# Optimization experiments

Hardware: AMD Instinct MI355X
Metric: run time of the kernel (lower is better)

## Reference

```python
import jax, jax.numpy as jnp
import numpy as np

N_NODES = 1_000_000
N_EDGES = 16_000_000
F_IN, F_H1, F_H2, N_CLS = 32, 16, 8, 5
N_GRAPHS = 10_000


def setup_inputs() -> dict:
    key = jax.random.key(0)
    ks = jax.random.split(key, 10)
    x = jax.random.normal(ks[0], (N_NODES, F_IN), dtype=jnp.float32)
    edge_index = jax.random.randint(ks[1], (2, N_EDGES), 0, N_NODES, dtype=jnp.int32)
    batch = jnp.sort(jax.random.randint(ks[2], (N_NODES,), 0, N_GRAPHS, dtype=jnp.int32))
    # learned params (Glorot-ish scale)
    W1 = jax.random.normal(ks[3], (F_IN, F_H1), dtype=jnp.float32) / np.sqrt(F_IN)
    b1 = jnp.zeros((F_H1,), dtype=jnp.float32)
    W2 = jax.random.normal(ks[4], (F_H1, F_H2), dtype=jnp.float32) / np.sqrt(F_H1)
    b2 = jnp.zeros((F_H2,), dtype=jnp.float32)
    Wl = jax.random.normal(ks[5], (F_H2, N_CLS), dtype=jnp.float32) / np.sqrt(F_H2)
    bl = jnp.zeros((N_CLS,), dtype=jnp.float32)
    return {"x": x, "edge_index": edge_index, "batch": batch, "num_graphs": N_GRAPHS,
            "W1": W1, "b1": b1, "W2": W2, "b2": b2, "Wl": Wl, "bl": bl}


def _gcn_conv(x, W, b, src, dst, deg_inv_sqrt, norm_e, num_nodes):
    # h = X W, then symmetric-normalized aggregation with self loops:
    # out_i = sum_{(j->i)} norm_ji * h_j + deg_i^{-1} * h_i + b
    h = x @ W                                  # [N, F_out]
    msg = h[src] * norm_e[:, None]             # [E, F_out] gather + scale
    agg = jax.ops.segment_sum(msg, dst, num_segments=num_nodes)
    self_loop = h * (deg_inv_sqrt * deg_inv_sqrt)[:, None]
    return agg + self_loop + b


def reference(x, edge_index, batch, num_graphs, W1, b1, W2, b2, Wl, bl):
    num_nodes = x.shape[0]
    src, dst = edge_index[0], edge_index[1]
    # degrees including self loops (GCN: A_hat = A + I)
    deg = jax.ops.segment_sum(jnp.ones_like(dst, dtype=x.dtype), dst,
                              num_segments=num_nodes) + 1.0
    deg_inv_sqrt = jax.lax.rsqrt(deg)
    norm_e = deg_inv_sqrt[src] * deg_inv_sqrt[dst]   # [E]

    h = _gcn_conv(x, W1, b1, src, dst, deg_inv_sqrt, norm_e, num_nodes)
    h = jax.nn.relu(h)
    h = _gcn_conv(h, W2, b2, src, dst, deg_inv_sqrt, norm_e, num_nodes)
    h = jax.nn.relu(h)

    # global_mean_pool over graph ids
    sums = jax.ops.segment_sum(h, batch, num_segments=num_graphs)     # [G, F_H2]
    cnts = jax.ops.segment_sum(jnp.ones((num_nodes,), dtype=h.dtype), batch,
                               num_segments=num_graphs)
    pooled = sums / jnp.maximum(cnts, 1.0)[:, None]
    return pooled @ Wl + bl
```

## Files before the change

### kernel.cpp

```cpp
#include <hip/hip_runtime.h>


namespace {

constexpr int F_IN = 32, F_H1 = 16, F_H2 = 8, N_CLS = 5;
constexpr int BB = 10, NPB = 1 << BB;
constexpr int MAXB = 1024;
constexpr int CHUNK = 12288;


__global__ void k_mm1(const float* __restrict__ x, const float* __restrict__ W,
                      const float* __restrict__ dis, float* __restrict__ h, int N) {
  __shared__ float w[F_IN * F_H1];
  for (int k = threadIdx.x; k < F_IN * F_H1; k += blockDim.x) w[k] = W[k];
  __syncthreads();
  int i = blockIdx.x * blockDim.x + threadIdx.x;
  if (i >= N) return;
  const float4* xr = reinterpret_cast<const float4*>(x + (size_t)i * F_IN);
  float acc[F_H1];
#pragma unroll
  for (int f = 0; f < F_H1; ++f) acc[f] = 0.f;
#pragma unroll
  for (int k4 = 0; k4 < F_IN / 4; ++k4) {
    float4 v = xr[k4];
    float vv[4] = {v.x, v.y, v.z, v.w};
#pragma unroll
    for (int j = 0; j < 4; ++j) {
      const float* wr = &w[(k4 * 4 + j) * F_H1];
#pragma unroll
      for (int f = 0; f < F_H1; ++f) acc[f] = fmaf(vv[j], wr[f], acc[f]);
    }
  }
  float s = dis ? dis[i] : 1.0f;
  float4* hr = reinterpret_cast<float4*>(h + (size_t)i * F_H1);
#pragma unroll
  for (int q = 0; q < F_H1 / 4; ++q)
    hr[q] = make_float4(s * acc[q * 4], s * acc[q * 4 + 1], s * acc[q * 4 + 2],
                        s * acc[q * 4 + 3]);
}

__global__ void k_mm2(const float* __restrict__ in, const float* __restrict__ W,
                      const float* __restrict__ dis, float* __restrict__ h, int N) {
  __shared__ float w[F_H1 * F_H2];
  for (int k = threadIdx.x; k < F_H1 * F_H2; k += blockDim.x) w[k] = W[k];
  __syncthreads();
  int i = blockIdx.x * blockDim.x + threadIdx.x;
  if (i >= N) return;
  const float4* xr = reinterpret_cast<const float4*>(in + (size_t)i * F_H1);
  float acc[F_H2];
#pragma unroll
  for (int f = 0; f < F_H2; ++f) acc[f] = 0.f;
#pragma unroll
  for (int k4 = 0; k4 < F_H1 / 4; ++k4) {
    float4 v = xr[k4];
    float vv[4] = {v.x, v.y, v.z, v.w};
#pragma unroll
    for (int j = 0; j < 4; ++j) {
      const float* wr = &w[(k4 * 4 + j) * F_H2];
#pragma unroll
      for (int f = 0; f < F_H2; ++f) acc[f] = fmaf(vv[j], wr[f], acc[f]);
    }
  }
  float s = dis ? dis[i] : 1.0f;
  float4* hr = reinterpret_cast<float4*>(h + (size_t)i * F_H2);
#pragma unroll
  for (int q = 0; q < F_H2 / 4; ++q)
    hr[q] = make_float4(s * acc[q * 4], s * acc[q * 4 + 1], s * acc[q * 4 + 2],
                        s * acc[q * 4 + 3]);
}

__global__ void k_final(const float* __restrict__ pooled, const float* __restrict__ cnts,
                        const float* __restrict__ Wl, const float* __restrict__ bl,
                        float* __restrict__ out, int total) {
  int gid = blockIdx.x * blockDim.x + threadIdx.x;
  if (gid >= total) return;
  int g = gid / N_CLS, c = gid % N_CLS;
  float s = 0.f;
#pragma unroll
  for (int f = 0; f < F_H2; ++f) s += pooled[g * F_H2 + f] * Wl[f * N_CLS + c];
  out[gid] = s / fmaxf(cnts[g], 1.f) + bl[c];
}


__global__ void k_hist(const int* __restrict__ dst, int* __restrict__ bcnt,
                       int E, int nbuck) {
  __shared__ int h[MAXB];
  for (int i = threadIdx.x; i < MAXB; i += blockDim.x) h[i] = 0;
  __syncthreads();
  for (int e = blockIdx.x * blockDim.x + threadIdx.x; e < E;
       e += gridDim.x * blockDim.x)
    atomicAdd(&h[dst[e] >> BB], 1);
  __syncthreads();
  for (int i = threadIdx.x; i < nbuck; i += blockDim.x)
    if (h[i]) atomicAdd(&bcnt[i], h[i]);
}

__global__ void k_bscan(const int* __restrict__ bcnt, int* __restrict__ bbase,
                        int* __restrict__ bcur, int nbuck, int E) {
  __shared__ int s[MAXB];
  int t = threadIdx.x;
  int v = (t < nbuck) ? bcnt[t] : 0;
  s[t] = v;
  __syncthreads();
  for (int off = 1; off < MAXB; off <<= 1) {
    int x = (t >= off) ? s[t - off] : 0;
    __syncthreads();
    s[t] += x;
    __syncthreads();
  }
  int ex = s[t] - v;
  if (t < nbuck) { bbase[t] = ex; bcur[t] = ex; }
  if (t == 0) bbase[nbuck] = E;
}

__global__ __launch_bounds__(256)
void k_binscatter(const int* __restrict__ dst, const int* __restrict__ src,
                  int* __restrict__ bcur, int* __restrict__ packed, int E) {
  __shared__ int hist[MAXB];
  __shared__ int sbase[MAXB];
  __shared__ int lcur[MAXB];
  __shared__ int stg[CHUNK];
  __shared__ int stmp[256];
  int t = threadIdx.x;
  int c0 = blockIdx.x * CHUNK;
  int n = min(CHUNK, E - c0);
  for (int i = t; i < MAXB; i += 256) hist[i] = 0;
  __syncthreads();
  for (int j = t; j < n; j += 256) atomicAdd(&hist[dst[c0 + j] >> BB], 1);
  __syncthreads();
  int v[4], sum = 0;
  int b4 = t * 4;
#pragma unroll
  for (int k = 0; k < 4; ++k) { v[k] = hist[b4 + k]; sum += v[k]; }
  stmp[t] = sum;
  __syncthreads();
  for (int off = 1; off < 256; off <<= 1) {
    int x = (t >= off) ? stmp[t - off] : 0;
    __syncthreads();
    stmp[t] += x;
    __syncthreads();
  }
  int run = stmp[t] - sum;
#pragma unroll
  for (int k = 0; k < 4; ++k) { sbase[b4 + k] = run; lcur[b4 + k] = run; run += v[k]; }
  __syncthreads();
  for (int i = t; i < MAXB; i += 256) {
    int c = hist[i];
    if (c) hist[i] = atomicAdd(&bcur[i], c);
  }
  __syncthreads();
  for (int j = t; j < n; j += 256) {
    int d = dst[c0 + j], s = src[c0 + j];
    int b = d >> BB;
    int p = atomicAdd(&lcur[b], 1);
    stg[p] = ((d & (NPB - 1)) << 20) | s;
  }
  __syncthreads();
  for (int j = t; j < n; j += 256) {
    int lo = 0, hi = MAXB - 1;
    while (lo < hi) {
      int mid = (lo + hi + 1) >> 1;
      if (sbase[mid] <= j) lo = mid; else hi = mid - 1;
    }
    packed[hist[lo] + (j - sbase[lo])] = stg[j];
  }
}

__global__ void k_dis_b(const int* __restrict__ bbase, const int* __restrict__ packed,
                        float* __restrict__ dis, int N) {
  __shared__ int cnt[NPB];
  int t = threadIdx.x;
  for (int i = t; i < NPB; i += blockDim.x) cnt[i] = 0;
  __syncthreads();
  int b = blockIdx.x;
  int beg = bbase[b], end = bbase[b + 1];
  for (int e = beg + t; e < end; e += blockDim.x)
    atomicAdd(&cnt[packed[e] >> 20], 1);
  __syncthreads();
  int node0 = b << BB;
  for (int i = t; i < NPB; i += blockDim.x) {
    int node = node0 + i;
    if (node < N) dis[node] = rsqrtf((float)cnt[i] + 1.0f);
  }
}


template <int F>
__global__ __launch_bounds__(512)
void k_conv(const int* __restrict__ bbase, const int* __restrict__ packed,
            const float* __restrict__ dis, const float* __restrict__ hs,
            const float* __restrict__ bias, float* __restrict__ out, int N) {
  __shared__ float acc[NPB * F];
  int t = threadIdx.x;
  for (int i = t; i < NPB * F; i += 512) acc[i] = 0.f;
  __syncthreads();
  int b = blockIdx.x;
  int beg = bbase[b], end = bbase[b + 1];
  const int EPI = 512 / F;
  int f = t % F, eg = t / F;
  constexpr int U = 8;
  int e = beg + eg;
  for (; e + (U - 1) * EPI < end; e += U * EPI) {
    int p[U];
    float m[U];
#pragma unroll
    for (int k = 0; k < U; ++k) p[k] = packed[e + k * EPI];
#pragma unroll
    for (int k = 0; k < U; ++k)
      m[k] = hs[(size_t)(p[k] & 0xFFFFF) * F + f];
#pragma unroll
    for (int k = 0; k < U; ++k)
      atomicAdd(&acc[(p[k] >> 20) * F + f], m[k]);
  }
  for (; e < end; e += EPI) {
    int p = packed[e];
    atomicAdd(&acc[(p >> 20) * F + f], hs[(size_t)(p & 0xFFFFF) * F + f]);
  }
  __syncthreads();
  int node0 = b << BB;
  for (int i = t; i < NPB * F; i += 512) {
    int node = node0 + i / F;
    if (node >= N) continue;
    int ff = i % F;
    float v = fmaf(dis[node], acc[i] + hs[(size_t)node * F + ff], bias[ff]);
    out[(size_t)node * F + ff] = fmaxf(v, 0.f);
  }
}

__global__ __launch_bounds__(512)
void k_conv_pool(const int* __restrict__ bbase, const int* __restrict__ packed,
                 const float* __restrict__ dis, const float* __restrict__ hs,
                 const float* __restrict__ bias, const int* __restrict__ batch,
                 float* __restrict__ pooled, float* __restrict__ cnts, int N, int G) {
  constexpr int F = F_H2;
  constexpr int GW = 32;
  __shared__ float acc[NPB * F];
  __shared__ float pacc[GW * F];
  __shared__ float pcnt[GW];
  __shared__ int gmin_s;
  int t = threadIdx.x;
  for (int i = t; i < NPB * F; i += 512) acc[i] = 0.f;
  for (int i = t; i < GW * F; i += 512) pacc[i] = 0.f;
  if (t < GW) pcnt[t] = 0.f;
  int b = blockIdx.x;
  int node0 = b << BB;
  if (t == 0) gmin_s = batch[node0];
  __syncthreads();
  int beg = bbase[b], end = bbase[b + 1];
  const int EPI = 512 / F;
  int f = t % F, eg = t / F;
  constexpr int U = 8;
  int e = beg + eg;
  for (; e + (U - 1) * EPI < end; e += U * EPI) {
    int p[U];
    float m[U];
#pragma unroll
    for (int k = 0; k < U; ++k) p[k] = packed[e + k * EPI];
#pragma unroll
    for (int k = 0; k < U; ++k)
      m[k] = hs[(size_t)(p[k] & 0xFFFFF) * F + f];
#pragma unroll
    for (int k = 0; k < U; ++k)
      atomicAdd(&acc[(p[k] >> 20) * F + f], m[k]);
  }
  for (; e < end; e += EPI) {
    int p = packed[e];
    atomicAdd(&acc[(p >> 20) * F + f], hs[(size_t)(p & 0xFFFFF) * F + f]);
  }
  __syncthreads();
  int gmin = gmin_s;
  for (int i = t; i < NPB * F; i += 512) {
    int node = node0 + i / F;
    if (node >= N) continue;
    int ff = i % F;
    float v = fmaf(dis[node], acc[i] + hs[(size_t)node * F + ff], bias[ff]);
    v = fmaxf(v, 0.f);
    int g = batch[node];
    int idx = g - gmin;
    if (idx < GW) {
      atomicAdd(&pacc[idx * F + ff], v);
      if (ff == 0) atomicAdd(&pcnt[idx], 1.0f);
    } else {
      atomicAdd(&pooled[g * F + ff], v);
      if (ff == 0) atomicAdd(&cnts[g], 1.0f);
    }
  }
  __syncthreads();
  for (int i = t; i < GW * F; i += 512) {
    int g = gmin + i / F;
    float v = pacc[i];
    if (g < G && v != 0.f) atomicAdd(&pooled[g * F + i % F], v);
  }
  if (t < GW) {
    int g = gmin + t;
    float c = pcnt[t];
    if (g < G && c > 0.f) atomicAdd(&cnts[g], c);
  }
}


__global__ void k_deg(const int* __restrict__ dst, float* __restrict__ deg, int E) {
  int e = blockIdx.x * blockDim.x + threadIdx.x;
  if (e < E) atomicAdd(&deg[dst[e]], 1.0f);
}
__global__ void k_dis(float* __restrict__ d, int N) {
  int i = blockIdx.x * blockDim.x + threadIdx.x;
  if (i < N) d[i] = rsqrtf(d[i] + 1.0f);
}
template <int F>
__global__ void k_edge(const int* __restrict__ src, const int* __restrict__ dst,
                       const float* __restrict__ dis, const float* __restrict__ h,
                       float* __restrict__ agg, int total) {
  int gid = blockIdx.x * blockDim.x + threadIdx.x;
  if (gid >= total) return;
  int e = gid / F, f = gid % F;
  int s = src[e], d = dst[e];
  atomicAdd(&agg[d * F + f], h[s * F + f] * dis[s] * dis[d]);
}
template <int F>
__global__ void k_combine(const float* __restrict__ h, const float* __restrict__ dis,
                          const float* __restrict__ b, float* __restrict__ agg, int total) {
  int gid = blockIdx.x * blockDim.x + threadIdx.x;
  if (gid >= total) return;
  int i = gid / F, f = gid % F;
  float di = dis[i];
  agg[gid] = fmaxf(agg[gid] + h[gid] * di * di + b[f], 0.f);
}
__global__ void k_combine_pool_fb(const float* __restrict__ h2, const float* __restrict__ agg2,
                                  const float* __restrict__ dis, const float* __restrict__ b,
                                  const int* __restrict__ batch, float* __restrict__ pooled,
                                  float* __restrict__ cnts, int total) {
  int gid = blockIdx.x * blockDim.x + threadIdx.x;
  if (gid >= total) return;
  int i = gid >> 3, f = gid & 7;
  float di = dis[i];
  float v = fmaxf(agg2[gid] + h2[gid] * di * di + b[f], 0.f);
  int g = batch[i];
  atomicAdd(&pooled[g * F_H2 + f], v);
  if (f == 0) atomicAdd(&cnts[g], 1.0f);
}

}

extern "C" void kernel_launch(void* const* d_in, const int* in_sizes, int n_in,
                              void* d_out, int out_size, void* d_ws, size_t ws_size,
                              hipStream_t stream) {
  const float* x   = (const float*)d_in[0];
  const int* ei    = (const int*)d_in[1];
  const int* batch = (const int*)d_in[2];
  const float* W1 = (const float*)d_in[4];
  const float* b1 = (const float*)d_in[5];
  const float* W2 = (const float*)d_in[6];
  const float* b2 = (const float*)d_in[7];
  const float* Wl = (const float*)d_in[8];
  const float* bl = (const float*)d_in[9];

  const int N = in_sizes[0] / F_IN;
  const int E = in_sizes[1] / 2;
  const int G = out_size / N_CLS;
  const int* src  = ei;
  const int* dstp = ei + E;

  const int BLK = 256;
  const int nbuck = (N + NPB - 1) >> BB;

  size_t need = (size_t)(3 * MAXB + 8) * 4
              + (size_t)E * 4
              + (size_t)N * 4
              + (size_t)N * F_H1 * 4
              + (size_t)N * F_H1 * 4
              + (size_t)G * (F_H2 + 1) * 4 + 1024;

  if (N <= (1 << 20) && nbuck <= MAXB && ws_size >= need) {
    char* p = (char*)d_ws;
    int*   bcnt   = (int*)p;    p += (size_t)MAXB * 4;
    int*   bbase  = (int*)p;    p += (size_t)(MAXB + 4) * 4;
    int*   bcur   = (int*)p;    p += (size_t)MAXB * 4;
    int*   packed = (int*)p;    p += (size_t)E * 4;
    float* dis    = (float*)p;  p += (size_t)N * 4;
    float* H      = (float*)p;  p += (size_t)N * F_H1 * 4;
    float* O      = (float*)p;  p += (size_t)N * F_H1 * 4;
    float* pooled = (float*)p;  p += (size_t)G * F_H2 * 4;
    float* cnts   = (float*)p;

    hipMemsetAsync(bcnt, 0, (size_t)MAXB * 4, stream);
    hipMemsetAsync(pooled, 0, ((size_t)G * F_H2 + G) * 4, stream);

    k_hist<<<2048, BLK, 0, stream>>>(dstp, bcnt, E, nbuck);
    k_bscan<<<1, MAXB, 0, stream>>>(bcnt, bbase, bcur, nbuck, E);
    k_binscatter<<<(E + CHUNK - 1) / CHUNK, BLK, 0, stream>>>(dstp, src, bcur, packed, E);
    k_dis_b<<<nbuck, BLK, 0, stream>>>(bbase, packed, dis, N);

    k_mm1<<<(N + BLK - 1) / BLK, BLK, 0, stream>>>(x, W1, dis, H, N);
    k_conv<F_H1><<<nbuck, 512, 0, stream>>>(bbase, packed, dis, H, b1, O, N);
    k_mm2<<<(N + BLK - 1) / BLK, BLK, 0, stream>>>(O, W2, dis, H, N);
    k_conv_pool<<<nbuck, 512, 0, stream>>>(bbase, packed, dis, H, b2, batch,
                                           pooled, cnts, N, G);

    k_final<<<(G * N_CLS + BLK - 1) / BLK, BLK, 0, stream>>>(
        pooled, cnts, Wl, bl, (float*)d_out, G * N_CLS);
    return;
  }

  float* ws = (float*)d_ws;
  float* dis    = ws;
  float* A      = ws + N;
  float* B      = A + (size_t)N * F_H1;
  float* h2     = A;
  float* agg2   = A + (size_t)N * F_H2;
  float* pooled = B + (size_t)N * F_H1;
  float* cnts   = pooled + (size_t)G * F_H2;

  hipMemsetAsync(dis, 0, (size_t)N * sizeof(float), stream);
  hipMemsetAsync(B, 0, (size_t)N * F_H1 * sizeof(float), stream);
  hipMemsetAsync(pooled, 0, ((size_t)G * F_H2 + G) * sizeof(float), stream);

  k_deg<<<(E + BLK - 1) / BLK, BLK, 0, stream>>>(dstp, dis, E);
  k_dis<<<(N + BLK - 1) / BLK, BLK, 0, stream>>>(dis, N);
  k_mm1<<<(N + BLK - 1) / BLK, BLK, 0, stream>>>(x, W1, nullptr, A, N);
  k_edge<F_H1><<<(E * F_H1 + BLK - 1) / BLK, BLK, 0, stream>>>(src, dstp, dis, A, B, E * F_H1);
  k_combine<F_H1><<<(N * F_H1 + BLK - 1) / BLK, BLK, 0, stream>>>(A, dis, b1, B, N * F_H1);
  hipMemsetAsync(agg2, 0, (size_t)N * F_H2 * sizeof(float), stream);
  k_mm2<<<(N + BLK - 1) / BLK, BLK, 0, stream>>>(B, W2, nullptr, h2, N);
  k_edge<F_H2><<<(E * F_H2 + BLK - 1) / BLK, BLK, 0, stream>>>(src, dstp, dis, h2, agg2, E * F_H2);
  k_combine_pool_fb<<<(N * F_H2 + BLK - 1) / BLK, BLK, 0, stream>>>(
      h2, agg2, dis, b2, batch, pooled, cnts, N * F_H2);
  k_final<<<(G * N_CLS + BLK - 1) / BLK, BLK, 0, stream>>>(
      pooled, cnts, Wl, bl, (float*)d_out, G * N_CLS);
}
```

Baseline: 3.345 ms.

## Bin edges by source and route gathered features to destination buckets

Edges are now binned by source bucket, so each routing block reads its source rows of H with locality. Each block scatters the gathered feature values into a staging buffer grouped by destination bucket, and a second accumulate kernel then sums them in shared memory per destination bucket, optionally in K passes sized to the workspace. Degree is computed separately with global integer atomics. This replaces the random gather of H in the conv kernels, but it writes and reads an E×F intermediate buffer, adds several kernels and histogram passes, and drops the old fallback path.

Result: slower. 7.889 ms (+135.9%).

```diff
diff --git a/kernel.cpp b/kernel.cpp
--- a/kernel.cpp
+++ b/kernel.cpp
@@ -7,6 +7,8 @@
 constexpr int BB = 10, NPB = 1 << BB;
 constexpr int MAXB = 1024;
 constexpr int CHUNK = 12288;
+constexpr int SUBC = 4096;
+constexpr int GW = 32;
 
 
 __global__ void k_mm1(const float* __restrict__ x, const float* __restrict__ W,
@@ -31,7 +33,7 @@
       for (int f = 0; f < F_H1; ++f) acc[f] = fmaf(vv[j], wr[f], acc[f]);
     }
   }
-  float s = dis ? dis[i] : 1.0f;
+  float s = dis[i];
   float4* hr = reinterpret_cast<float4*>(h + (size_t)i * F_H1);
 #pragma unroll
   for (int q = 0; q < F_H1 / 4; ++q)
@@ -61,7 +63,7 @@
       for (int f = 0; f < F_H2; ++f) acc[f] = fmaf(vv[j], wr[f], acc[f]);
     }
   }
-  float s = dis ? dis[i] : 1.0f;
+  float s = dis[i];
   float4* hr = reinterpret_cast<float4*>(h + (size_t)i * F_H2);
 #pragma unroll
   for (int q = 0; q < F_H2 / 4; ++q)
@@ -82,14 +84,24 @@
 }
 
 
-__global__ void k_hist(const int* __restrict__ dst, int* __restrict__ bcnt,
+__global__ void k_deg_i(const int* __restrict__ dst, int* __restrict__ deg, int E) {
+  int e = blockIdx.x * blockDim.x + threadIdx.x;
+  if (e < E) atomicAdd(&deg[dst[e]], 1);
+}
+__global__ void k_dis_i(const int* __restrict__ deg, float* __restrict__ dis, int N) {
+  int i = blockIdx.x * blockDim.x + threadIdx.x;
+  if (i < N) dis[i] = rsqrtf((float)deg[i] + 1.0f);
+}
+
+
+__global__ void k_hist(const int* __restrict__ key, int* __restrict__ bcnt,
                        int E, int nbuck) {
   __shared__ int h[MAXB];
   for (int i = threadIdx.x; i < MAXB; i += blockDim.x) h[i] = 0;
   __syncthreads();
   for (int e = blockIdx.x * blockDim.x + threadIdx.x; e < E;
        e += gridDim.x * blockDim.x)
-    atomicAdd(&h[dst[e] >> BB], 1);
+    atomicAdd(&h[key[e] >> BB], 1);
   __syncthreads();
   for (int i = threadIdx.x; i < nbuck; i += blockDim.x)
     if (h[i]) atomicAdd(&bcnt[i], h[i]);
@@ -114,7 +126,7 @@
 }
 
 __global__ __launch_bounds__(256)
-void k_binscatter(const int* __restrict__ dst, const int* __restrict__ src,
+void k_binscatter(const int* __restrict__ key, const int* __restrict__ payload,
                   int* __restrict__ bcur, int* __restrict__ packed, int E) {
   __shared__ int hist[MAXB];
   __shared__ int sbase[MAXB];
@@ -126,7 +138,7 @@
   int n = min(CHUNK, E - c0);
   for (int i = t; i < MAXB; i += 256) hist[i] = 0;
   __syncthreads();
-  for (int j = t; j < n; j += 256) atomicAdd(&hist[dst[c0 + j] >> BB], 1);
+  for (int j = t; j < n; j += 256) atomicAdd(&hist[key[c0 + j] >> BB], 1);
   __syncthreads();
   int v[4], sum = 0;
   int b4 = t * 4;
@@ -150,10 +162,10 @@
   }
   __syncthreads();
   for (int j = t; j < n; j += 256) {
-    int d = dst[c0 + j], s = src[c0 + j];
-    int b = d >> BB;
+    int kk = key[c0 + j], pl = payload[c0 + j];
+    int b = kk >> BB;
     int p = atomicAdd(&lcur[b], 1);
-    stg[p] = ((d & (NPB - 1)) << 20) | s;
+    stg[p] = ((kk & (NPB - 1)) << 20) | pl;
   }
   __syncthreads();
   for (int j = t; j < n; j += 256) {
@@ -166,21 +178,188 @@
   }
 }
 
-__global__ void k_dis_b(const int* __restrict__ bbase, const int* __restrict__ packed,
-                        float* __restrict__ dis, int N) {
-  __shared__ int cnt[NPB];
+
+__global__ void k_vcur_init(int* __restrict__ vcur, const int* __restrict__ bbase_d,
+                            int rs, int re) {
+  int i = rs + threadIdx.x;
+  if (i < re) vcur[i] = bbase_d[i];
+}
+
+template <int F>
+__global__ __launch_bounds__(512)
+void k_route(const int* __restrict__ bbase_s, const int* __restrict__ packed_s,
+             const float* __restrict__ hs, int* __restrict__ vcur,
+             const int* __restrict__ bbase_d, float* __restrict__ val,
+             int* __restrict__ dIdx, int rs, int re) {
+  __shared__ int hist[MAXB];
+  __shared__ int sbase[MAXB];
+  __shared__ int lcur[MAXB];
+  __shared__ int stg[SUBC];
+  __shared__ int spos[SUBC];
+  __shared__ int stmp[512];
   int t = threadIdx.x;
-  for (int i = t; i < NPB; i += blockDim.x) cnt[i] = 0;
-  __syncthreads();
-  int b = blockIdx.x;
-  int beg = bbase[b], end = bbase[b + 1];
-  for (int e = beg + t; e < end; e += blockDim.x)
-    atomicAdd(&cnt[packed[e] >> 20], 1);
-  __syncthreads();
+  int sb = blockIdx.x;
+  int beg = bbase_s[sb], endAll = bbase_s[sb + 1];
+  int srcbase = sb << BB;
+  int base0 = bbase_d[rs];
+  int W = re - rs;
+  const int GPB = 512 / F;
+  int f = t % F, g = t / F;
+
+  for (int c0 = beg; c0 < endAll; c0 += SUBC) {
+    int n = min(SUBC, endAll - c0);
+    int pe[SUBC / 512];
+    int nIt = (n + 511) / 512;
+#pragma unroll
+    for (int it = 0; it < SUBC / 512; ++it) {
+      int j = it * 512 + t;
+      pe[it] = (it < nIt && j < n) ? packed_s[c0 + j] : 0;
+    }
+    for (int i = t; i < W; i += 512) hist[i] = 0;
+    __syncthreads();
+    for (int it = 0; it < nIt; ++it) {
+      int j = it * 512 + t;
+      if (j < n) {
+        int b = (pe[it] & 0xFFFFF) >> BB;
+        if (b >= rs && b < re) atomicAdd(&hist[b - rs], 1);
+      }
+    }
+    __syncthreads();
+    int v0 = (2 * t < W) ? hist[2 * t] : 0;
+    int v1 = (2 * t + 1 < W) ? hist[2 * t + 1] : 0;
+    int sum = v0 + v1;
+    stmp[t] = sum;
+    __syncthreads();
+    for (int off = 1; off < 512; off <<= 1) {
+      int x = (t >= off) ? stmp[t - off] : 0;
+      __syncthreads();
+      stmp[t] += x;
+      __syncthreads();
+    }
+    int run = stmp[t] - sum;
+    if (2 * t < W) { sbase[2 * t] = run; lcur[2 * t] = run; }
+    if (2 * t + 1 < W) { sbase[2 * t + 1] = run + v0; lcur[2 * t + 1] = run + v0; }
+    __syncthreads();
+    for (int i = t; i < W; i += 512) {
+      int c = hist[i];
+      if (c) hist[i] = atomicAdd(&vcur[rs + i], c);
+    }
+    __syncthreads();
+    for (int it = 0; it < nIt; ++it) {
+      int j = it * 512 + t;
+      if (j < n) {
+        int p = pe[it];
+        int b = (p & 0xFFFFF) >> BB;
+        if (b >= rs && b < re) {
+          int q = atomicAdd(&lcur[b - rs], 1);
+          stg[q] = p;
+        }
+      }
+    }
+    __syncthreads();
+    int m = stmp[511];
+    for (int j = t; j < m; j += 512) {
+      int lo = 0, hi = W - 1;
+      while (lo < hi) {
+        int mid = (lo + hi + 1) >> 1;
+        if (sbase[mid] <= j) lo = mid; else hi = mid - 1;
+      }
+      spos[j] = hist[lo] + (j - sbase[lo]) - base0;
+    }
+    __syncthreads();
+    for (int j = g; j < m; j += GPB) {
+      int p = stg[j];
+      int sL = p >> 20;
+      int dL = p & (NPB - 1);
+      int pos = spos[j];
+      val[(size_t)pos * F + f] = hs[(size_t)(srcbase + sL) * F + f];
+      if (f == 0) dIdx[pos] = dL;
+    }
+    __syncthreads();
+  }
+}
+
+
+template <int F, bool POOL>
+__global__ __launch_bounds__(512)
+void k_accum(const int* __restrict__ bbase_d, const int* __restrict__ dIdx,
+             const float* __restrict__ val, const float* __restrict__ dis,
+             const float* __restrict__ hs, const float* __restrict__ bias,
+             const int* __restrict__ batch, float* __restrict__ out,
+             float* __restrict__ pooled, float* __restrict__ cnts,
+             int rs, int N, int G) {
+  __shared__ float acc[NPB * F];
+  __shared__ float pacc[GW * F_H2];
+  __shared__ float pcnt[GW];
+  __shared__ int gmin_s;
+  int t = threadIdx.x;
+  int b = rs + blockIdx.x;
   int node0 = b << BB;
-  for (int i = t; i < NPB; i += blockDim.x) {
-    int node = node0 + i;
-    if (node < N) dis[node] = rsqrtf((float)cnt[i] + 1.0f);
+  for (int i = t; i < NPB * F; i += 512) acc[i] = 0.f;
+  if (POOL) {
+    for (int i = t; i < GW * F_H2; i += 512) pacc[i] = 0.f;
+    if (t < GW) pcnt[t] = 0.f;
+    if (t == 0) gmin_s = batch[min(node0, N - 1)];
+  }
+  __syncthreads();
+  int beg = bbase_d[b], end = bbase_d[b + 1], base0 = bbase_d[rs];
+  const int GPB = 512 / F;
+  int f = t % F, g = t / F;
+  int e = beg + g;
+  for (; e + 3 * GPB < end; e += 4 * GPB) {
+    int p0 = e - base0, p1 = p0 + GPB, p2 = p1 + GPB, p3 = p2 + GPB;
+    int d0 = dIdx[p0], d1 = dIdx[p1], d2 = dIdx[p2], d3 = dIdx[p3];
+    float v0 = val[(size_t)p0 * F + f];
+    float v1 = val[(size_t)p1 * F + f];
+    float v2 = val[(size_t)p2 * F + f];
+    float v3 = val[(size_t)p3 * F + f];
+    atomicAdd(&acc[d0 * F + f], v0);
+    atomicAdd(&acc[d1 * F + f], v1);
+    atomicAdd(&acc[d2 * F + f], v2);
+    atomicAdd(&acc[d3 * F + f], v3);
+  }
+  for (; e < end; e += GPB) {
+    int p = e - base0;
+    atomicAdd(&acc[dIdx[p] * F + f], val[(size_t)p * F + f]);
+  }
+  __syncthreads();
+  if (!POOL) {
+    for (int i = t; i < NPB * F; i += 512) {
+      int node = node0 + i / F;
+      if (node >= N) continue;
+      int ff = i % F;
+      float v = fmaf(dis[node], acc[i] + hs[(size_t)node * F + ff], bias[ff]);
+      out[(size_t)node * F + ff] = fmaxf(v, 0.f);
+    }
+  } else {
+    int gmin = gmin_s;
+    for (int i = t; i < NPB * F; i += 512) {
+      int node = node0 + i / F;
+      if (node >= N) continue;
+      int ff = i % F;
+      float v = fmaf(dis[node], acc[i] + hs[(size_t)node * F + ff], bias[ff]);
+      v = fmaxf(v, 0.f);
+      int gr = batch[node];
+      int idx = gr - gmin;
+      if (idx >= 0 && idx < GW) {
+        atomicAdd(&pacc[idx * F_H2 + ff], v);
+        if (ff == 0) atomicAdd(&pcnt[idx], 1.0f);
+      } else {
+        atomicAdd(&pooled[gr * F_H2 + ff], v);
+        if (ff == 0) atomicAdd(&cnts[gr], 1.0f);
+      }
+    }
+    __syncthreads();
+    for (int i = t; i < GW * F_H2; i += 512) {
+      int gr = gmin + i / F_H2;
+      float v = pacc[i];
+      if (gr < G && v != 0.f) atomicAdd(&pooled[gr * F_H2 + i % F_H2], v);
+    }
+    if (t < GW) {
+      int gr = gmin + t;
+      float c = pcnt[t];
+      if (gr < G && c > 0.f) atomicAdd(&cnts[gr], c);
+    }
   }
 }
 
@@ -206,11 +385,9 @@
 #pragma unroll
     for (int k = 0; k < U; ++k) p[k] = packed[e + k * EPI];
 #pragma unroll
-    for (int k = 0; k < U; ++k)
-      m[k] = hs[(size_t)(p[k] & 0xFFFFF) * F + f];
-#pragma unroll
-    for (int k = 0; k < U; ++k)
-      atomicAdd(&acc[(p[k] >> 20) * F + f], m[k]);
+    for (int k = 0; k < U; ++k) m[k] = hs[(size_t)(p[k] & 0xFFFFF) * F + f];
+#pragma unroll
+    for (int k = 0; k < U; ++k) atomicAdd(&acc[(p[k] >> 20) * F + f], m[k]);
   }
   for (; e < end; e += EPI) {
     int p = packed[e];
@@ -233,7 +410,6 @@
                  const float* __restrict__ bias, const int* __restrict__ batch,
                  float* __restrict__ pooled, float* __restrict__ cnts, int N, int G) {
   constexpr int F = F_H2;
-  constexpr int GW = 32;
   __shared__ float acc[NPB * F];
   __shared__ float pacc[GW * F];
   __shared__ float pcnt[GW];
@@ -244,7 +420,7 @@
   if (t < GW) pcnt[t] = 0.f;
   int b = blockIdx.x;
   int node0 = b << BB;
-  if (t == 0) gmin_s = batch[node0];
+  if (t == 0) gmin_s = batch[min(node0, N - 1)];
   __syncthreads();
   int beg = bbase[b], end = bbase[b + 1];
   const int EPI = 512 / F;
@@ -257,11 +433,9 @@
 #pragma unroll
     for (int k = 0; k < U; ++k) p[k] = packed[e + k * EPI];
 #pragma unroll
-    for (int k = 0; k < U; ++k)
-      m[k] = hs[(size_t)(p[k] & 0xFFFFF) * F + f];
-#pragma unroll
-    for (int k = 0; k < U; ++k)
-      atomicAdd(&acc[(p[k] >> 20) * F + f], m[k]);
+    for (int k = 0; k < U; ++k) m[k] = hs[(size_t)(p[k] & 0xFFFFF) * F + f];
+#pragma unroll
+    for (int k = 0; k < U; ++k) atomicAdd(&acc[(p[k] >> 20) * F + f], m[k]);
   }
   for (; e < end; e += EPI) {
     int p = packed[e];
@@ -275,69 +449,27 @@
     int ff = i % F;
     float v = fmaf(dis[node], acc[i] + hs[(size_t)node * F + ff], bias[ff]);
     v = fmaxf(v, 0.f);
-    int g = batch[node];
-    int idx = g - gmin;
-    if (idx < GW) {
+    int gr = batch[node];
+    int idx = gr - gmin;
+    if (idx >= 0 && idx < GW) {
       atomicAdd(&pacc[idx * F + ff], v);
       if (ff == 0) atomicAdd(&pcnt[idx], 1.0f);
     } else {
-      atomicAdd(&pooled[g * F + ff], v);
-      if (ff == 0) atomicAdd(&cnts[g], 1.0f);
+      atomicAdd(&pooled[gr * F + ff], v);
+      if (ff == 0) atomicAdd(&cnts[gr], 1.0f);
     }
   }
   __syncthreads();
   for (int i = t; i < GW * F; i += 512) {
-    int g = gmin + i / F;
+    int gr = gmin + i / F;
     float v = pacc[i];
-    if (g < G && v != 0.f) atomicAdd(&pooled[g * F + i % F], v);
+    if (gr < G && v != 0.f) atomicAdd(&pooled[gr * F + i % F], v);
   }
   if (t < GW) {
-    int g = gmin + t;
+    int gr = gmin + t;
     float c = pcnt[t];
-    if (g < G && c > 0.f) atomicAdd(&cnts[g], c);
-  }
-}
-
-
-__global__ void k_deg(const int* __restrict__ dst, float* __restrict__ deg, int E) {
-  int e = blockIdx.x * blockDim.x + threadIdx.x;
-  if (e < E) atomicAdd(&deg[dst[e]], 1.0f);
-}
-__global__ void k_dis(float* __restrict__ d, int N) {
-  int i = blockIdx.x * blockDim.x + threadIdx.x;
-  if (i < N) d[i] = rsqrtf(d[i] + 1.0f);
-}
-template <int F>
-__global__ void k_edge(const int* __restrict__ src, const int* __restrict__ dst,
-                       const float* __restrict__ dis, const float* __restrict__ h,
-                       float* __restrict__ agg, int total) {
-  int gid = blockIdx.x * blockDim.x + threadIdx.x;
-  if (gid >= total) return;
-  int e = gid / F, f = gid % F;
-  int s = src[e], d = dst[e];
-  atomicAdd(&agg[d * F + f], h[s * F + f] * dis[s] * dis[d]);
-}
-template <int F>
-__global__ void k_combine(const float* __restrict__ h, const float* __restrict__ dis,
-                          const float* __restrict__ b, float* __restrict__ agg, int total) {
-  int gid = blockIdx.x * blockDim.x + threadIdx.x;
-  if (gid >= total) return;
-  int i = gid / F, f = gid % F;
-  float di = dis[i];
-  agg[gid] = fmaxf(agg[gid] + h[gid] * di * di + b[f], 0.f);
-}
-__global__ void k_combine_pool_fb(const float* __restrict__ h2, const float* __restrict__ agg2,
-                                  const float* __restrict__ dis, const float* __restrict__ b,
-                                  const int* __restrict__ batch, float* __restrict__ pooled,
-                                  float* __restrict__ cnts, int total) {
-  int gid = blockIdx.x * blockDim.x + threadIdx.x;
-  if (gid >= total) return;
-  int i = gid >> 3, f = gid & 7;
-  float di = dis[i];
-  float v = fmaxf(agg2[gid] + h2[gid] * di * di + b[f], 0.f);
-  int g = batch[i];
-  atomicAdd(&pooled[g * F_H2 + f], v);
-  if (f == 0) atomicAdd(&cnts[g], 1.0f);
+    if (gr < G && c > 0.f) atomicAdd(&cnts[gr], c);
+  }
 }
 
 }
@@ -364,67 +496,86 @@
   const int BLK = 256;
   const int nbuck = (N + NPB - 1) >> BB;
 
-  size_t need = (size_t)(3 * MAXB + 8) * 4
-              + (size_t)E * 4
-              + (size_t)N * 4
-              + (size_t)N * F_H1 * 4
-              + (size_t)N * F_H1 * 4
-              + (size_t)G * (F_H2 + 1) * 4 + 1024;
-
-  if (N <= (1 << 20) && nbuck <= MAXB && ws_size >= need) {
-    char* p = (char*)d_ws;
-    int*   bcnt   = (int*)p;    p += (size_t)MAXB * 4;
-    int*   bbase  = (int*)p;    p += (size_t)(MAXB + 4) * 4;
-    int*   bcur   = (int*)p;    p += (size_t)MAXB * 4;
-    int*   packed = (int*)p;    p += (size_t)E * 4;
-    float* dis    = (float*)p;  p += (size_t)N * 4;
-    float* H      = (float*)p;  p += (size_t)N * F_H1 * 4;
-    float* O      = (float*)p;  p += (size_t)N * F_H1 * 4;
-    float* pooled = (float*)p;  p += (size_t)G * F_H2 * 4;
-    float* cnts   = (float*)p;
-
-    hipMemsetAsync(bcnt, 0, (size_t)MAXB * 4, stream);
-    hipMemsetAsync(pooled, 0, ((size_t)G * F_H2 + G) * 4, stream);
-
-    k_hist<<<2048, BLK, 0, stream>>>(dstp, bcnt, E, nbuck);
-    k_bscan<<<1, MAXB, 0, stream>>>(bcnt, bbase, bcur, nbuck, E);
-    k_binscatter<<<(E + CHUNK - 1) / CHUNK, BLK, 0, stream>>>(dstp, src, bcur, packed, E);
-    k_dis_b<<<nbuck, BLK, 0, stream>>>(bbase, packed, dis, N);
+  size_t fixed = (size_t)(6 * MAXB + 16) * 4
+               + (size_t)N * 4
+               + (size_t)N * 4
+               + (size_t)E * 4
+               + (size_t)N * F_H1 * 4
+               + (size_t)N * F_H1 * 4
+               + (size_t)G * (F_H2 + 1) * 4 + 1024;
+
+  int K = 0;
+  size_t cap = 0;
+  for (int k = 1; k <= 16; k <<= 1) {
+    size_t c = (k == 1) ? (size_t)E : (size_t)E / k + (size_t)E / (k * 4) + 65536;
+    size_t need = fixed + c * 4 + c * F_H1 * 4;
+    if (need <= ws_size) { K = k; cap = c; break; }
+  }
+
+  char* p = (char*)d_ws;
+  int*   bcnt_d  = (int*)p;   p += (size_t)MAXB * 4;
+  int*   bbase_d = (int*)p;   p += (size_t)(MAXB + 8) * 4;
+  int*   bcur_d  = (int*)p;   p += (size_t)MAXB * 4;
+  int*   bcnt_s  = (int*)p;   p += (size_t)MAXB * 4;
+  int*   bbase_s = (int*)p;   p += (size_t)(MAXB + 8) * 4;
+  int*   bcur_s  = (int*)p;   p += (size_t)MAXB * 4;
+  int*   deg     = (int*)p;   p += (size_t)N * 4;
+  float* dis     = (float*)p; p += (size_t)N * 4;
+  int*   packed  = (int*)p;   p += (size_t)E * 4;
+  float* H       = (float*)p; p += (size_t)N * F_H1 * 4;
+  float* O       = (float*)p; p += (size_t)N * F_H1 * 4;
+  float* pooled  = (float*)p; p += (size_t)G * F_H2 * 4;
+  float* cnts    = (float*)p; p += (size_t)G * 4;
+  int*   dIdx    = (int*)p;   p += cap * 4;
+  float* val     = (float*)p;
+
+  hipMemsetAsync(deg, 0, (size_t)N * 4, stream);
+  hipMemsetAsync(bcnt_d, 0, (size_t)MAXB * 4, stream);
+  hipMemsetAsync(bcnt_s, 0, (size_t)MAXB * 4, stream);
+  hipMemsetAsync(pooled, 0, ((size_t)G * F_H2 + G) * 4, stream);
+
+  k_deg_i<<<(E + BLK - 1) / BLK, BLK, 0, stream>>>(dstp, deg, E);
+  k_dis_i<<<(N + BLK - 1) / BLK, BLK, 0, stream>>>(deg, dis, N);
+  k_hist<<<2048, BLK, 0, stream>>>(dstp, bcnt_d, E, nbuck);
+  k_bscan<<<1, MAXB, 0, stream>>>(bcnt_d, bbase_d, bcur_d, nbuck, E);
+
+  if (K > 0) {
+    k_hist<<<2048, BLK, 0, stream>>>(src, bcnt_s, E, nbuck);
+    k_bscan<<<1, MAXB, 0, stream>>>(bcnt_s, bbase_s, bcur_s, nbuck, E);
+    k_binscatter<<<(E + CHUNK - 1) / CHUNK, BLK, 0, stream>>>(src, dstp, bcur_s,
+                                                              packed, E);
+    const int Wk = (nbuck + K - 1) / K;
 
     k_mm1<<<(N + BLK - 1) / BLK, BLK, 0, stream>>>(x, W1, dis, H, N);
-    k_conv<F_H1><<<nbuck, 512, 0, stream>>>(bbase, packed, dis, H, b1, O, N);
+    for (int pp = 0; pp < K; ++pp) {
+      int rs = pp * Wk, re = min(rs + Wk, nbuck);
+      if (rs >= re) break;
+      k_vcur_init<<<1, MAXB, 0, stream>>>(bcur_d, bbase_d, rs, re);
+      k_route<F_H1><<<nbuck, 512, 0, stream>>>(bbase_s, packed, H, bcur_d,
+                                               bbase_d, val, dIdx, rs, re);
+      k_accum<F_H1, false><<<re - rs, 512, 0, stream>>>(
+          bbase_d, dIdx, val, dis, H, b1, batch, O, nullptr, nullptr, rs, N, G);
+    }
     k_mm2<<<(N + BLK - 1) / BLK, BLK, 0, stream>>>(O, W2, dis, H, N);
-    k_conv_pool<<<nbuck, 512, 0, stream>>>(bbase, packed, dis, H, b2, batch,
+    for (int pp = 0; pp < K; ++pp) {
+      int rs = pp * Wk, re = min(rs + Wk, nbuck);
+      if (rs >= re) break;
+      k_vcur_init<<<1, MAXB, 0, stream>>>(bcur_d, bbase_d, rs, re);
+      k_route<F_H2><<<nbuck, 512, 0, stream>>>(bbase_s, packed, H, bcur_d,
+                                               bbase_d, val, dIdx, rs, re);
+      k_accum<F_H2, true><<<re - rs, 512, 0, stream>>>(
+          bbase_d, dIdx, val, dis, H, b2, batch, nullptr, pooled, cnts, rs, N, G);
+    }
+  } else {
+    k_binscatter<<<(E + CHUNK - 1) / CHUNK, BLK, 0, stream>>>(dstp, src, bcur_d,
+                                                              packed, E);
+    k_mm1<<<(N + BLK - 1) / BLK, BLK, 0, stream>>>(x, W1, dis, H, N);
+    k_conv<F_H1><<<nbuck, 512, 0, stream>>>(bbase_d, packed, dis, H, b1, O, N);
+    k_mm2<<<(N + BLK - 1) / BLK, BLK, 0, stream>>>(O, W2, dis, H, N);
+    k_conv_pool<<<nbuck, 512, 0, stream>>>(bbase_d, packed, dis, H, b2, batch,
                                            pooled, cnts, N, G);
-
-    k_final<<<(G * N_CLS + BLK - 1) / BLK, BLK, 0, stream>>>(
-        pooled, cnts, Wl, bl, (float*)d_out, G * N_CLS);
-    return;
-  }
-
-  float* ws = (float*)d_ws;
-  float* dis    = ws;
-  float* A      = ws + N;
-  float* B      = A + (size_t)N * F_H1;
-  float* h2     = A;
-  float* agg2   = A + (size_t)N * F_H2;
-  float* pooled = B + (size_t)N * F_H1;
-  float* cnts   = pooled + (size_t)G * F_H2;
-
-  hipMemsetAsync(dis, 0, (size_t)N * sizeof(float), stream);
-  hipMemsetAsync(B, 0, (size_t)N * F_H1 * sizeof(float), stream);
-  hipMemsetAsync(pooled, 0, ((size_t)G * F_H2 + G) * sizeof(float), stream);
-
-  k_deg<<<(E + BLK - 1) / BLK, BLK, 0, stream>>>(dstp, dis, E);
-  k_dis<<<(N + BLK - 1) / BLK, BLK, 0, stream>>>(dis, N);
-  k_mm1<<<(N + BLK - 1) / BLK, BLK, 0, stream>>>(x, W1, nullptr, A, N);
-  k_edge<F_H1><<<(E * F_H1 + BLK - 1) / BLK, BLK, 0, stream>>>(src, dstp, dis, A, B, E * F_H1);
-  k_combine<F_H1><<<(N * F_H1 + BLK - 1) / BLK, BLK, 0, stream>>>(A, dis, b1, B, N * F_H1);
-  hipMemsetAsync(agg2, 0, (size_t)N * F_H2 * sizeof(float), stream);
-  k_mm2<<<(N + BLK - 1) / BLK, BLK, 0, stream>>>(B, W2, nullptr, h2, N);
-  k_edge<F_H2><<<(E * F_H2 + BLK - 1) / BLK, BLK, 0, stream>>>(src, dstp, dis, h2, agg2, E * F_H2);
-  k_combine_pool_fb<<<(N * F_H2 + BLK - 1) / BLK, BLK, 0, stream>>>(
-      h2, agg2, dis, b2, batch, pooled, cnts, N * F_H2);
+  }
+
   k_final<<<(G * N_CLS + BLK - 1) / BLK, BLK, 0, stream>>>(
       pooled, cnts, Wl, bl, (float*)d_out, G * N_CLS);
 }
```
